# Optimization experiments

Hardware: AMD Instinct MI355X
Metric: run time of the kernel (lower is better)

The kernel has to match this reference:

```python
import jax, jax.numpy as jnp
import numpy as np

N = 16384
INPUT_DIM = 256
HIDDEN1 = 128
HIDDEN2 = 64


def setup_inputs() -> dict:
    key = jax.random.key(0)
    ks = jax.random.split(key, 8)
    X = jax.random.normal(ks[0], (N, INPUT_DIM), dtype=jnp.float32)
    adj = jax.random.uniform(ks[1], (N, N), dtype=jnp.float32)
    # Xavier-uniform style scaling for weights
    def xavier(k, shape):
        fan_in, fan_out = shape
        lim = float(np.sqrt(6.0 / (fan_in + fan_out)))
        return jax.random.uniform(k, shape, dtype=jnp.float32, minval=-lim, maxval=lim)
    W1 = xavier(ks[2], (INPUT_DIM, HIDDEN1))
    Wm = xavier(ks[3], (HIDDEN1, HIDDEN2))
    Ws = xavier(ks[4], (HIDDEN1, HIDDEN2))
    Wp = xavier(ks[5], (HIDDEN2, HIDDEN2))
    bp = jnp.zeros((HIDDEN2,), dtype=jnp.float32)
    noise = jax.random.normal(ks[6], (N, HIDDEN2), dtype=jnp.float32)
    return {"X": X, "adj": adj, "W1": W1, "Wm": Wm, "Ws": Ws,
            "Wp": Wp, "bp": bp, "noise": noise}


def _gcn(x, adj, W, activation):
    # GraphConvSparse: adj @ (x @ W) then activation
    h = adj @ (x @ W)
    return activation(h)


def reference(X, adj, W1, Wm, Ws, Wp, bp, noise):
    # base GCN with ReLU
    hidden = _gcn(X, adj, W1, jax.nn.relu)            # [N, hidden1]
    # mean branch: identity-activation GCN then Linear projection
    Z = _gcn(hidden, adj, Wm, lambda x: x)            # [N, hidden2]
    mean = Z @ Wp + bp                                # [N, hidden2]
    # logstd branch with clamp(max=10)
    logstd = _gcn(hidden, adj, Ws, lambda x: x)
    logstd = jnp.minimum(logstd, 10.0)
    # reparameterization trick
    sampled_z = noise * jnp.exp(logstd) + mean        # [N, hidden2]
    return sampled_z
```

## Files before the change

### kernel.cpp

```cpp
#include <hip/hip_runtime.h>


typedef __bf16 bf16_t;
typedef __attribute__((ext_vector_type(4))) __bf16 bf16x4;
typedef __attribute__((ext_vector_type(8))) __bf16 bf16x8;
typedef __attribute__((ext_vector_type(16))) float f32x16;
typedef __attribute__((ext_vector_type(4)))  float f32x4;

#define N_NODES 16384
#define MFMA3(ACC, A, B) \
    ACC = __builtin_amdgcn_mfma_f32_32x32x16_bf16(A, B, ACC, 0, 0, 0)

__device__ __forceinline__ int frag_off(int r, int c) {
    int K16  = r >> 4;
    int cblk = c >> 5;
    int g    = (r >> 3) & 1;
    int lane = (c & 31) + (g << 5);
    return ((K16 * 4 + cblk) << 9) + (lane << 3) + (r & 7);
}

__device__ __forceinline__ float4 relu_add4(float4 a, float4 b) {
    float4 r;
    r.x = fmaxf(a.x + b.x, 0.f); r.y = fmaxf(a.y + b.y, 0.f);
    r.z = fmaxf(a.z + b.z, 0.f); r.w = fmaxf(a.w + b.w, 0.f);
    return r;
}

template<int K, bool FUSED, bool ADD2>
__global__ __launch_bounds__(256)
void producer_kernel(const float* __restrict__ A,
                     const float* __restrict__ A2,
                     const float* __restrict__ W,
                     const float* __restrict__ Wa,
                     const float* __restrict__ Wb,
                     bf16_t* __restrict__ Bh,
                     bf16_t* __restrict__ Bl)
{
    __shared__ float As[32][128];
    __shared__ float Wsh[32][128];
    const int t    = threadIdx.x;
    const int row0 = blockIdx.x * 128;
    const int tc   = t & 15, tr = t >> 4;

    float acc[8][8];
    #pragma unroll
    for (int i = 0; i < 8; ++i)
        #pragma unroll
        for (int j = 0; j < 8; ++j) acc[i][j] = 0.f;

    const int ra = t >> 1, ks = (t & 1) << 4;
    const int wk = t >> 3, wc = (t & 7) << 4;

    for (int k0 = 0; k0 < K; k0 += 32) {
        const float* ap = A + (size_t)(row0 + ra) * K + k0 + ks;
        float4 a0 = *(const float4*)(ap);
        float4 a1 = *(const float4*)(ap + 4);
        float4 a2 = *(const float4*)(ap + 8);
        float4 a3 = *(const float4*)(ap + 12);
        if (ADD2) {
            const float* ap2 = A2 + (size_t)(row0 + ra) * K + k0 + ks;
            a0 = relu_add4(a0, *(const float4*)(ap2));
            a1 = relu_add4(a1, *(const float4*)(ap2 + 4));
            a2 = relu_add4(a2, *(const float4*)(ap2 + 8));
            a3 = relu_add4(a3, *(const float4*)(ap2 + 12));
        }
        float4 w0, w1, w2, w3;
        if (!FUSED) {
            const float* wp = W + (size_t)(k0 + wk) * 128 + wc;
            w0 = *(const float4*)(wp);     w1 = *(const float4*)(wp + 4);
            w2 = *(const float4*)(wp + 8); w3 = *(const float4*)(wp + 12);
        } else {
            const float* wp = (wc < 64) ? (Wa + (size_t)(k0 + wk) * 64 + wc)
                                        : (Wb + (size_t)(k0 + wk) * 64 + (wc - 64));
            w0 = *(const float4*)(wp);     w1 = *(const float4*)(wp + 4);
            w2 = *(const float4*)(wp + 8); w3 = *(const float4*)(wp + 12);
        }
        __syncthreads();
        {
            float tmp[16] = {a0.x,a0.y,a0.z,a0.w, a1.x,a1.y,a1.z,a1.w,
                             a2.x,a2.y,a2.z,a2.w, a3.x,a3.y,a3.z,a3.w};
            #pragma unroll
            for (int j = 0; j < 16; ++j) As[ks + j][ra] = tmp[j];
            *(float4*)&Wsh[wk][wc     ] = w0;
            *(float4*)&Wsh[wk][wc +  4] = w1;
            *(float4*)&Wsh[wk][wc +  8] = w2;
            *(float4*)&Wsh[wk][wc + 12] = w3;
        }
        __syncthreads();
        #pragma unroll 4
        for (int k = 0; k < 32; ++k) {
            float av[8], wv[8];
            *(float4*)&av[0] = *(const float4*)&As[k][8 * tr];
            *(float4*)&av[4] = *(const float4*)&As[k][8 * tr + 4];
            *(float4*)&wv[0] = *(const float4*)&Wsh[k][8 * tc];
            *(float4*)&wv[4] = *(const float4*)&Wsh[k][8 * tc + 4];
            #pragma unroll
            for (int i = 0; i < 8; ++i)
                #pragma unroll
                for (int j = 0; j < 8; ++j)
                    acc[i][j] = fmaf(av[i], wv[j], acc[i][j]);
        }
    }

    #pragma unroll
    for (int i = 0; i < 8; ++i) {
        int r = row0 + 8 * tr + i;
        #pragma unroll
        for (int j = 0; j < 8; ++j) {
            int c = 8 * tc + j;
            float v = acc[i][j];
            bf16_t h = (bf16_t)v;
            bf16_t l = (bf16_t)(v - (float)h);
            int off = frag_off(r, c);
            Bh[off] = h;
            Bl[off] = l;
        }
    }
}

struct BSet { bf16x8 h[4]; bf16x8 l[4]; };

__global__ __launch_bounds__(512, 4)
void adj_gemm_kernel(const float* __restrict__ adj,
                     const bf16_t* __restrict__ Bh,
                     const bf16_t* __restrict__ Bl,
                     float* __restrict__ P0,
                     float* __restrict__ P1)
{
    __shared__ __align__(16) bf16_t AsH[64 * 256];
    __shared__ __align__(16) bf16_t AsL[64 * 256];
    const int t    = threadIdx.x;
    const int lane = t & 63;
    const int w    = t >> 6;
    const int mt   = blockIdx.x >> 1;
    const int kh   = blockIdx.x & 1;
    const int row0 = mt << 6;
    const int hi32 = lane >> 5;
    float* const outP = kh ? P1 : P0;

    const float* aBase = adj + (size_t)(row0 + (w << 3)) * 16384
                             + (kh << 13) + (lane << 2);

    int wIdx[8];
    #pragma unroll
    for (int j = 0; j < 8; ++j) {
        int row = (w << 3) + j;
        wIdx[j] = (row << 8) + ((((lane >> 2) ^ (row & 15)) << 4)
                                + ((lane & 3) << 2));
    }

    const int rh    = w >> 2, cq = w & 3;
    const int frow  = (rh << 5) + (lane & 31);
    const int rbase = (frow << 8) + (hi32 << 3);
    const int rx    = frow & 15;

    const int tb   = (cq << 9) + (lane << 3);
    const int sub0 = kh << 7;

    f32x16 acc;
    #pragma unroll
    for (int i = 0; i < 16; ++i) acc[i] = 0.f;

    f32x4 ar[8];
    BSet S;

    auto loadAdj = [&](int mac) {
        const float* p = aBase + (mac << 8);
        #pragma unroll
        for (int j = 0; j < 8; ++j)
            ar[j] = __builtin_nontemporal_load((const f32x4*)(p + (size_t)j * 16384));
    };
    auto cvtWrite = [&]() {
        #pragma unroll
        for (int j = 0; j < 8; ++j) {
            bf16x4 hv, lv;
            #pragma unroll
            for (int e = 0; e < 4; ++e) {
                float v = ar[j][e];
                bf16_t h = (bf16_t)v;
                hv[e] = h;
                lv[e] = (bf16_t)(v - (float)h);
            }
            *(bf16x4*)&AsH[wIdx[j]] = hv;
            *(bf16x4*)&AsL[wIdx[j]] = lv;
        }
    };
    auto loadB = [&](int sub) {
        const size_t base = ((size_t)sub << 13) + tb;
        #pragma unroll
        for (int s = 0; s < 4; ++s) {
            S.h[s] = *(const bf16x8*)(Bh + base + (s << 11));
            S.l[s] = *(const bf16x8*)(Bl + base + (s << 11));
        }
    };
    auto computeS = [&](int s) {
        #pragma unroll
        for (int k16 = 0; k16 < 4; ++k16) {
            const int u  = (s << 2) + k16;
            const int id = rbase + ((u ^ rx) << 4);
            bf16x8 ah = *(const bf16x8*)&AsH[id];
            bf16x8 al = *(const bf16x8*)&AsL[id];
            MFMA3(acc, ah, S.h[k16]);
            MFMA3(acc, ah, S.l[k16]);
            MFMA3(acc, al, S.h[k16]);
        }
    };

#define SYNC_LDS() do { asm volatile("s_waitcnt lgkmcnt(0)" ::: "memory"); \
                        __builtin_amdgcn_s_barrier(); } while (0)

    loadAdj(0);
    for (int m = 0; m < 32; ++m) {
        cvtWrite();
        SYNC_LDS();
        const int sb = sub0 + (m << 2);
        loadB(sb + 0);
        if (m < 31) loadAdj(m + 1);
        computeS(0);
        loadB(sb + 1);  computeS(1);
        loadB(sb + 2);  computeS(2);
        loadB(sb + 3);  computeS(3);
        SYNC_LDS();
    }
#undef SYNC_LDS

    const int col = (cq << 5) + (lane & 31);
    const int rb  = row0 + (rh << 5) + (hi32 << 2);
    #pragma unroll
    for (int q = 0; q < 16; ++q) {
        int r = rb + (q & 3) + ((q >> 2) << 3);
        outP[(size_t)r * 128 + col] = acc[q];
    }
}

__global__ __launch_bounds__(256)
void final_kernel(const float* __restrict__ T0,
                  const float* __restrict__ T1,
                  const float* __restrict__ Wp,
                  const float* __restrict__ bp,
                  const float* __restrict__ noise,
                  float* __restrict__ out)
{
    __shared__ float Wps[64][64];
    __shared__ float Ts[64][64];
    const int t = threadIdx.x;
    const int row0 = blockIdx.x * 64;
    {
        int k = t >> 2, c0 = (t & 3) << 4;
        #pragma unroll
        for (int i = 0; i < 4; ++i)
            *(float4*)&Wps[k][c0 + 4 * i] = *(const float4*)&Wp[(size_t)k * 64 + c0 + 4 * i];
        #pragma unroll
        for (int i = 0; i < 4; ++i) {
            float4 z0 = *(const float4*)&T0[(size_t)(row0 + k) * 128 + c0 + 4 * i];
            float4 z1 = *(const float4*)&T1[(size_t)(row0 + k) * 128 + c0 + 4 * i];
            float4 zs; zs.x = z0.x + z1.x; zs.y = z0.y + z1.y;
            zs.z = z0.z + z1.z; zs.w = z0.w + z1.w;
            *(float4*)&Ts[k][c0 + 4 * i] = zs;
        }
    }
    __syncthreads();

    const int r  = t >> 2;
    const int c0 = (t & 3) << 4;
    float acc[16];
    #pragma unroll
    for (int j = 0; j < 16; ++j) acc[j] = bp[c0 + j];
    for (int k = 0; k < 64; ++k) {
        float a = Ts[r][k];
        #pragma unroll
        for (int j = 0; j < 16; ++j) acc[j] = fmaf(a, Wps[k][c0 + j], acc[j]);
    }
    const int grow = row0 + r;
    #pragma unroll
    for (int j = 0; j < 16; ++j) {
        size_t li = (size_t)grow * 128 + 64 + c0 + j;
        float ls = T0[li] + T1[li];
        ls = fminf(ls, 10.0f);
        out[(size_t)grow * 64 + c0 + j] =
            noise[(size_t)grow * 64 + c0 + j] * __expf(ls) + acc[j];
    }
}

extern "C" void kernel_launch(void* const* d_in, const int* in_sizes, int n_in,
                              void* d_out, int out_size, void* d_ws, size_t ws_size,
                              hipStream_t stream) {
    const float* X     = (const float*)d_in[0];
    const float* adj   = (const float*)d_in[1];
    const float* W1    = (const float*)d_in[2];
    const float* Wm    = (const float*)d_in[3];
    const float* Wsv   = (const float*)d_in[4];
    const float* Wp    = (const float*)d_in[5];
    const float* bp    = (const float*)d_in[6];
    const float* noise = (const float*)d_in[7];
    float* out = (float*)d_out;

    char* ws = (char*)d_ws;
    bf16_t* Bh = (bf16_t*)ws;
    bf16_t* Bl = (bf16_t*)(ws + (4u << 20));
    float*  P0 = (float*)(ws + (8u << 20));
    float*  P1 = (float*)(ws + (16u << 20));

    producer_kernel<256, false, false><<<128, 256, 0, stream>>>(
        X, nullptr, W1, nullptr, nullptr, Bh, Bl);
    adj_gemm_kernel<<<512, 512, 0, stream>>>(adj, Bh, Bl, P0, P1);
    producer_kernel<128, true, true><<<128, 256, 0, stream>>>(
        P0, P1, nullptr, Wm, Wsv, Bh, Bl);
    adj_gemm_kernel<<<512, 512, 0, stream>>>(adj, Bh, Bl, P0, P1);
    final_kernel<<<256, 256, 0, stream>>>(P0, P1, Wp, bp, noise, out);
}
```

Baseline: 719.1 us.

## Warp-specialize adj GEMM into loader and MFMA waves with double-buffered LDS

The adjacency GEMM block grows to 12 waves. Four producer waves stream adj rows, split them into bf16 hi/lo, and write into a double-buffered LDS tile. Eight consumer waves run the MFMA loop on the other buffer, with ping-pong prefetch of the B fragments. The aim is to overlap global loads and conversion with tensor-core work. The cost is twice the LDS per block, which likely allows only one block per CU, and more registers in the producer waves.

New measurement: 732.6 us. Within noise of the previous version (+1.9%).

```diff
diff --git a/kernel.cpp b/kernel.cpp
--- a/kernel.cpp
+++ b/kernel.cpp
@@ -120,15 +120,15 @@
 
 struct BSet { bf16x8 h[4]; bf16x8 l[4]; };
 
-__global__ __launch_bounds__(512, 4)
+__global__ __launch_bounds__(768, 3)
 void adj_gemm_kernel(const float* __restrict__ adj,
                      const bf16_t* __restrict__ Bh,
                      const bf16_t* __restrict__ Bl,
                      float* __restrict__ P0,
                      float* __restrict__ P1)
 {
-    __shared__ __align__(16) bf16_t AsH[64 * 256];
-    __shared__ __align__(16) bf16_t AsL[64 * 256];
+    __shared__ __align__(16) bf16_t AsH[2][64 * 256];
+    __shared__ __align__(16) bf16_t AsL[2][64 * 256];
     const int t    = threadIdx.x;
     const int lane = t & 63;
     const int w    = t >> 6;
@@ -138,99 +138,119 @@
     const int hi32 = lane >> 5;
     float* const outP = kh ? P1 : P0;
 
-    const float* aBase = adj + (size_t)(row0 + (w << 3)) * 16384
-                             + (kh << 13) + (lane << 2);
-
-    int wIdx[8];
-    #pragma unroll
-    for (int j = 0; j < 8; ++j) {
-        int row = (w << 3) + j;
-        wIdx[j] = (row << 8) + ((((lane >> 2) ^ (row & 15)) << 4)
-                                + ((lane & 3) << 2));
-    }
-
-    const int rh    = w >> 2, cq = w & 3;
-    const int frow  = (rh << 5) + (lane & 31);
-    const int rbase = (frow << 8) + (hi32 << 3);
-    const int rx    = frow & 15;
-
-    const int tb   = (cq << 9) + (lane << 3);
-    const int sub0 = kh << 7;
-
-    f32x16 acc;
-    #pragma unroll
-    for (int i = 0; i < 16; ++i) acc[i] = 0.f;
-
-    f32x4 ar[8];
-    BSet S;
-
-    auto loadAdj = [&](int mac) {
-        const float* p = aBase + (mac << 8);
-        #pragma unroll
-        for (int j = 0; j < 8; ++j)
-            ar[j] = __builtin_nontemporal_load((const f32x4*)(p + (size_t)j * 16384));
-    };
-    auto cvtWrite = [&]() {
-        #pragma unroll
-        for (int j = 0; j < 8; ++j) {
-            bf16x4 hv, lv;
-            #pragma unroll
-            for (int e = 0; e < 4; ++e) {
-                float v = ar[j][e];
-                bf16_t h = (bf16_t)v;
-                hv[e] = h;
-                lv[e] = (bf16_t)(v - (float)h);
-            }
-            *(bf16x4*)&AsH[wIdx[j]] = hv;
-            *(bf16x4*)&AsL[wIdx[j]] = lv;
-        }
-    };
-    auto loadB = [&](int sub) {
-        const size_t base = ((size_t)sub << 13) + tb;
-        #pragma unroll
-        for (int s = 0; s < 4; ++s) {
-            S.h[s] = *(const bf16x8*)(Bh + base + (s << 11));
-            S.l[s] = *(const bf16x8*)(Bl + base + (s << 11));
-        }
-    };
-    auto computeS = [&](int s) {
-        #pragma unroll
-        for (int k16 = 0; k16 < 4; ++k16) {
-            const int u  = (s << 2) + k16;
-            const int id = rbase + ((u ^ rx) << 4);
-            bf16x8 ah = *(const bf16x8*)&AsH[id];
-            bf16x8 al = *(const bf16x8*)&AsL[id];
-            MFMA3(acc, ah, S.h[k16]);
-            MFMA3(acc, ah, S.l[k16]);
-            MFMA3(acc, al, S.h[k16]);
-        }
-    };
-
 #define SYNC_LDS() do { asm volatile("s_waitcnt lgkmcnt(0)" ::: "memory"); \
                         __builtin_amdgcn_s_barrier(); } while (0)
 
-    loadAdj(0);
-    for (int m = 0; m < 32; ++m) {
-        cvtWrite();
+    if (w < 4) {
+        const float* aBase = adj + (size_t)(row0 + (w << 4)) * 16384
+                                 + (kh << 13) + (lane << 2);
+        int wIdx[16];
+        #pragma unroll
+        for (int j = 0; j < 16; ++j) {
+            int row = (w << 4) + j;
+            wIdx[j] = (row << 8) + ((((lane >> 2) ^ (row & 15)) << 4)
+                                    + ((lane & 3) << 2));
+        }
+        f32x4 ar[16];
+
+        auto loadAdj = [&](int mac) {
+            const float* p = aBase + (mac << 8);
+            #pragma unroll
+            for (int j = 0; j < 16; ++j)
+                ar[j] = __builtin_nontemporal_load(
+                            (const f32x4*)(p + (size_t)j * 16384));
+        };
+        auto cvtWrite = [&](int buf) {
+            bf16_t* const H = &AsH[buf][0];
+            bf16_t* const L = &AsL[buf][0];
+            #pragma unroll
+            for (int j = 0; j < 16; ++j) {
+                bf16x4 hv, lv;
+                #pragma unroll
+                for (int e = 0; e < 4; ++e) {
+                    float v = ar[j][e];
+                    bf16_t h = (bf16_t)v;
+                    hv[e] = h;
+                    lv[e] = (bf16_t)(v - (float)h);
+                }
+                *(bf16x4*)&H[wIdx[j]] = hv;
+                *(bf16x4*)&L[wIdx[j]] = lv;
+            }
+        };
+
+        loadAdj(0);
+        cvtWrite(0);
+        loadAdj(1);
         SYNC_LDS();
-        const int sb = sub0 + (m << 2);
-        loadB(sb + 0);
-        if (m < 31) loadAdj(m + 1);
-        computeS(0);
-        loadB(sb + 1);  computeS(1);
-        loadB(sb + 2);  computeS(2);
-        loadB(sb + 3);  computeS(3);
+        for (int m = 0; m < 32; ++m) {
+            if (m < 31) cvtWrite((m + 1) & 1);
+            if (m < 30) loadAdj(m + 2);
+            SYNC_LDS();
+        }
+    } else {
+        const int cw = w - 4;
+        const int rh = cw >> 2, cq = cw & 3;
+        const int frow  = (rh << 5) + (lane & 31);
+        const int rbase = (frow << 8) + (hi32 << 3);
+        const int rx    = frow & 15;
+        const int tb    = (cq << 9) + (lane << 3);
+        const int sub0  = kh << 7;
+
+        f32x16 acc;
+        #pragma unroll
+        for (int i = 0; i < 16; ++i) acc[i] = 0.f;
+
+        BSet E, O;
+
+        auto loadB = [&](BSet& S, int sub) {
+            const size_t base = ((size_t)sub << 13) + tb;
+            #pragma unroll
+            for (int s = 0; s < 4; ++s) {
+                S.h[s] = *(const bf16x8*)(Bh + base + (s << 11));
+                S.l[s] = *(const bf16x8*)(Bl + base + (s << 11));
+            }
+        };
+        auto computeS = [&](int buf, const BSet& S, int s) {
+            const bf16_t* const H = &AsH[buf][0];
+            const bf16_t* const L = &AsL[buf][0];
+            #pragma unroll
+            for (int k16 = 0; k16 < 4; ++k16) {
+                const int u  = (s << 2) + k16;
+                const int id = rbase + ((u ^ rx) << 4);
+                bf16x8 ah = *(const bf16x8*)&H[id];
+                bf16x8 al = *(const bf16x8*)&L[id];
+                MFMA3(acc, ah, S.h[k16]);
+                MFMA3(acc, ah, S.l[k16]);
+                MFMA3(acc, al, S.h[k16]);
+            }
+        };
+
+        loadB(E, sub0);
+        loadB(O, sub0 + 1);
         SYNC_LDS();
+        for (int m = 0; m < 32; ++m) {
+            const int buf = m & 1;
+            const int sb  = sub0 + (m << 2);
+            computeS(buf, E, 0);
+            loadB(E, sb + 2);
+            computeS(buf, O, 1);
+            loadB(O, sb + 3);
+            computeS(buf, E, 2);
+            if (m < 31) loadB(E, sb + 4);
+            computeS(buf, O, 3);
+            if (m < 31) loadB(O, sb + 5);
+            SYNC_LDS();
+        }
+
+        const int col = (cq << 5) + (lane & 31);
+        const int rb  = row0 + (rh << 5) + (hi32 << 2);
+        #pragma unroll
+        for (int q = 0; q < 16; ++q) {
+            int r = rb + (q & 3) + ((q >> 2) << 3);
+            outP[(size_t)r * 128 + col] = acc[q];
+        }
     }
 #undef SYNC_LDS
-
-    const int col = (cq << 5) + (lane & 31);
-    const int rb  = row0 + (rh << 5) + (hi32 << 2);
-    #pragma unroll
-    for (int q = 0; q < 16; ++q) {
-        int r = rb + (q & 3) + ((q >> 2) << 3);
-        outP[(size_t)r * 128 + col] = acc[q];
-    }
 }
 
 __global__ __launch_bounds__(256)
@@ -303,9 +323,9 @@
 
     producer_kernel<256, false, false><<<128, 256, 0, stream>>>(
         X, nullptr, W1, nullptr, nullptr, Bh, Bl);
-    adj_gemm_kernel<<<512, 512, 0, stream>>>(adj, Bh, Bl, P0, P1);
+    adj_gemm_kernel<<<512, 768, 0, stream>>>(adj, Bh, Bl, P0, P1);
     producer_kernel<128, true, true><<<128, 256, 0, stream>>>(
         P0, P1, nullptr, Wm, Wsv, Bh, Bl);
-    adj_gemm_kernel<<<512, 512, 0, stream>>>(adj, Bh, Bl, P0, P1);
+    adj_gemm_kernel<<<512, 768, 0, stream>>>(adj, Bh, Bl, P0, P1);
     final_kernel<<<256, 256, 0, stream>>>(P0, P1, Wp, bp, noise, out);
 }
```
